# Performance work log

Hardware: AMD Instinct MI355X
Metric: run time of the kernel (lower is better)

The kernel has to match this reference:

```python
import jax, jax.numpy as jnp
import numpy as np

B, T, D = 2, 2048, 1280
H = 20
DH = D // H  # 64
S_PAST = 2048


def setup_inputs() -> dict:
    key = jax.random.key(0)
    ks = jax.random.split(key, 7)
    return {
        "x": jax.random.normal(ks[0], (B, T, D), dtype=jnp.float32),
        "past_K": jax.random.normal(ks[1], (B, H, S_PAST, DH), dtype=jnp.float32),
        "past_V": jax.random.normal(ks[2], (B, H, S_PAST, DH), dtype=jnp.float32),
        "w_q": jax.random.normal(ks[3], (D, D), dtype=jnp.float32),
        "w_k": jax.random.normal(ks[4], (D, D), dtype=jnp.float32),
        "w_v": jax.random.normal(ks[5], (D, D), dtype=jnp.float32),
        "W_o": jax.random.normal(ks[6], (D, D), dtype=jnp.float32),
    }


def reference(x, past_K, past_V, w_q, w_k, w_v, W_o):
    b, t, _ = x.shape
    # projections
    q = x @ w_q  # [B,T,D]
    k = x @ w_k
    v = x @ w_v
    # split heads -> [B,H,T,DH]
    Q = q.reshape(b, t, H, DH).transpose(0, 2, 1, 3)
    K = k.reshape(b, t, H, DH).transpose(0, 2, 1, 3)
    V = v.reshape(b, t, H, DH).transpose(0, 2, 1, 3)
    # concat KV cache along sequence dim
    K = jnp.concatenate([past_K, K], axis=-2)  # [B,H,S_past+T,DH]
    V = jnp.concatenate([past_V, V], axis=-2)
    # attention (no causal mask, matching the original module)
    scores = jnp.einsum("bhtd,bhsd->bhts", Q, K) / jnp.sqrt(jnp.float32(DH))
    attn = jax.nn.softmax(scores, axis=-1)
    values = jnp.einsum("bhts,bhsd->bhtd", attn, V)  # [B,H,T,DH]
    values = values.transpose(0, 2, 1, 3).reshape(b, t, D)
    out = values @ W_o
    return out, K, V
```

## Files before the change

### kernel.cpp

```cpp
#include <hip/hip_runtime.h>

#define NB 2
#define NH 20
#define TT 2048
#define DD 1280
#define DHH 64
#define SP 2048
#define SS 4096
#define MM (NB*TT)

typedef __attribute__((ext_vector_type(8))) short bf16x8;
typedef __attribute__((ext_vector_type(4))) float f32x4;
typedef unsigned short u16;
typedef unsigned int u32;

__device__ __forceinline__ f32x4 mfma16(bf16x8 a, bf16x8 b, f32x4 c) {
  return __builtin_amdgcn_mfma_f32_16x16x32_bf16(a, b, c, 0, 0, 0);
}

__device__ __forceinline__ u16 f2bf(float f) {
  u32 x = __builtin_bit_cast(u32, f);
  x += 0x7fffu + ((x >> 16) & 1u);
  return (u16)(x >> 16);
}
__device__ __forceinline__ float bf2f(u16 u) {
  u32 x = ((u32)u) << 16;
  return __builtin_bit_cast(float, x);
}

__device__ __forceinline__ float fexp2(float x) {
#if __has_builtin(__builtin_amdgcn_exp2f)
  return __builtin_amdgcn_exp2f(x);
#else
  return exp2f(x);
#endif
}

__device__ __forceinline__ u32 cvtpk(float lo, float hi) {
  u32 r;
  asm("v_cvt_pk_bf16_f32 %0, %1, %2" : "=v"(r) : "v"(lo), "v"(hi));
  return r;
}

__device__ __forceinline__ float vmax3(float a, float b, float c) {
  float d;
  asm("v_max3_f32 %0, %1, %2, %3" : "=v"(d) : "v"(a), "v"(b), "v"(c));
  return d;
}
__device__ __forceinline__ float max16(const f32x4* st) {
  float m0 = vmax3(st[0][0], st[0][1], st[0][2]);
  float m1 = vmax3(st[0][3], st[1][0], st[1][1]);
  float m2 = vmax3(st[1][2], st[1][3], st[2][0]);
  float m3 = vmax3(st[2][1], st[2][2], st[2][3]);
  float m4 = vmax3(st[3][0], st[3][1], st[3][2]);
  float m5 = vmax3(m0, m1, st[3][3]);
  float m6 = vmax3(m2, m3, m4);
  return fmaxf(m5, m6);
}

#define VMCNT0() asm volatile("s_waitcnt vmcnt(0)" ::: "memory")
#define BAR() __builtin_amdgcn_s_barrier()

template<int ROWS>
__device__ __forceinline__ void stage_swz(char* lds, const u16* __restrict__ gsrc,
                                          int ld, int tid) {
  constexpr int ITER = ROWS * 8 / 256;
#pragma unroll
  for (int i = 0; i < ITER; ++i) {
    int id = i * 256 + tid;
    int row = id >> 3, c = id & 7;
    int cs = c ^ (row & 7);
    const u16* src = gsrc + row * ld + cs * 8;
    __builtin_amdgcn_global_load_lds(
        (const __attribute__((address_space(1))) u32*)src,
        (__attribute__((address_space(3))) u32*)(lds + id * 16), 16, 0, 0);
  }
}

__device__ __forceinline__ void gload16(const u16* src, char* ldst) {
  __builtin_amdgcn_global_load_lds(
      (const __attribute__((address_space(1))) u32*)src,
      (__attribute__((address_space(3))) u32*)ldst, 16, 0, 0);
}

__device__ __forceinline__ bf16x8 frag_swz(const char* lds, int row, int cc) {
  return *(const bf16x8*)(lds + row * 128 + ((cc ^ (row & 7)) << 4));
}
__device__ __forceinline__ bf16x8 frag32(const char* lds, int row, int cc) {
  return *(const bf16x8*)(lds + row * 64 + ((cc ^ (row & 3)) << 4));
}

__global__ void splitx(const float* __restrict__ x, u16* __restrict__ xh,
                       u16* __restrict__ xl) {
  int i = blockIdx.x * 256 + threadIdx.x;
  float4 v = ((const float4*)x)[i];
  ushort4 hi, lo;
  hi.x = f2bf(v.x); lo.x = f2bf(v.x - bf2f(hi.x));
  hi.y = f2bf(v.y); lo.y = f2bf(v.y - bf2f(hi.y));
  hi.z = f2bf(v.z); lo.z = f2bf(v.z - bf2f(hi.z));
  hi.w = f2bf(v.w); lo.w = f2bf(v.w - bf2f(hi.w));
  ((ushort4*)xh)[i] = hi;
  ((ushort4*)xl)[i] = lo;
}

__global__ void transw(const float* __restrict__ wq, const float* __restrict__ wk,
                       const float* __restrict__ wv, const float* __restrict__ wo,
                       u16* __restrict__ wqkvh, u16* __restrict__ wqkvl,
                       u16* __restrict__ wot) {
  __shared__ float tile[64][65];
  int mat = blockIdx.z;
  const float* src = mat == 0 ? wq : mat == 1 ? wk : mat == 2 ? wv : wo;
  int k0 = blockIdx.x * 64, n0 = blockIdx.y * 64;
  int tid = threadIdx.x;
#pragma unroll
  for (int rep = 0; rep < 16; ++rep) {
    int id = rep * 256 + tid;
    int kl = id >> 6, nl = id & 63;
    tile[nl][kl] = src[(k0 + kl) * DD + n0 + nl];
  }
  __syncthreads();
#pragma unroll
  for (int rep = 0; rep < 16; ++rep) {
    int id = rep * 256 + tid;
    int nl = id >> 6, kl = id & 63;
    float v = tile[nl][kl];
    u16 hi = f2bf(v);
    if (mat < 3) {
      int idx = (mat * DD + n0 + nl) * DD + k0 + kl;
      wqkvh[idx] = hi;
      wqkvl[idx] = f2bf(v - bf2f(hi));
    } else {
      wot[(n0 + nl) * DD + k0 + kl] = hi;
    }
  }
}

__global__ void pastk(const float* __restrict__ pK, float* __restrict__ dK,
                      u16* __restrict__ Kh, u16* __restrict__ Kl) {
  int i = blockIdx.x * 256 + threadIdx.x;
  int e = i * 4;
  int dh = e & 63;
  int s = (e >> 6) & (SP - 1);
  int bh = e >> 17;
  float4 v = *(const float4*)(pK + e);
  int o = (bh * SS + s) * DHH + dh;
  *(float4*)(dK + o) = v;
  ushort4 hi, lo;
  hi.x = f2bf(v.x); lo.x = f2bf(v.x - bf2f(hi.x));
  hi.y = f2bf(v.y); lo.y = f2bf(v.y - bf2f(hi.y));
  hi.z = f2bf(v.z); lo.z = f2bf(v.z - bf2f(hi.z));
  hi.w = f2bf(v.w); lo.w = f2bf(v.w - bf2f(hi.w));
  *(ushort4*)(Kh + o) = hi;
  *(ushort4*)(Kl + o) = lo;
}

__global__ void pastv(const float* __restrict__ pV, float* __restrict__ dV,
                      u16* __restrict__ Vt) {
  __shared__ u16 tile[64][72];
  int bi = blockIdx.x;
  int bh = bi >> 5, st = bi & 31;
  int s0 = st * 64;
  int tid = threadIdx.x;
  const float* src = pV + (bh * SP + s0) * DHH;
  float* dst = dV + (bh * SS + s0) * DHH;
#pragma unroll
  for (int rep = 0; rep < 16; ++rep) {
    int id = rep * 256 + tid;
    int sl = id >> 6, dh = id & 63;
    float v = src[sl * DHH + dh];
    dst[sl * DHH + dh] = v;
    tile[dh][sl] = f2bf(v);
  }
  __syncthreads();
  u16* vdst = Vt + (bh * DHH) * SS + s0;
#pragma unroll
  for (int rep = 0; rep < 4; ++rep) {
    int id = rep * 256 + tid;
    int dh = id >> 4, s4 = (id & 15) * 4;
    ushort4 vv;
    vv.x = tile[dh][s4];     vv.y = tile[dh][s4 + 1];
    vv.z = tile[dh][s4 + 2]; vv.w = tile[dh][s4 + 3];
    *(ushort4*)(vdst + dh * SS + s4) = vv;
  }
}

__launch_bounds__(256, 2)
__global__ void gemm_qkv(const u16* __restrict__ xh, const u16* __restrict__ xl,
                         const u16* __restrict__ wh, const u16* __restrict__ wl,
                         u16* __restrict__ Qh, u16* __restrict__ Ql,
                         u16* __restrict__ Kh, u16* __restrict__ Kl,
                         u16* __restrict__ Vt,
                         float* __restrict__ dK, float* __restrict__ dV) {
  __shared__ __align__(16) char sm[65536];
  int tid = threadIdx.x, lane = tid & 63, w = tid >> 6;
  int wm = w >> 1, wn = w & 1;
  int r15 = lane & 15, grp = lane >> 4;
  int mBase = blockIdx.x * 128;
  int by = blockIdx.y;
  int nGlob = by * 128;
  const bool split = (by < 20);
  f32x4 acc[4][4] = {};
  int id0 = tid, id1 = 256 + tid;
  int r0 = id0 >> 2, c0 = id0 & 3;
  int r1 = id1 >> 2, c1 = id1 & 3;
  int so0 = r0 * DD + (c0 ^ (r0 & 3)) * 8;
  int so1 = r1 * DD + (c1 ^ (r1 & 3)) * 8;
  const u16* aH = xh + mBase * DD;
  const u16* aL = xl + mBase * DD;
  const u16* bH = wh + nGlob * DD;
  const u16* bL = wl + nGlob * DD;
  int do0 = id0 * 16, do1 = id1 * 16;

  auto stage = [&](int buf, int k0) {
    char* b = sm + buf * 32768;
    gload16(aH + k0 + so0, b + do0);
    gload16(aH + k0 + so1, b + do1);
    gload16(bH + k0 + so0, b + 16384 + do0);
    gload16(bH + k0 + so1, b + 16384 + do1);
    if (split) {
      gload16(aL + k0 + so0, b + 8192 + do0);
      gload16(aL + k0 + so1, b + 8192 + do1);
      gload16(bL + k0 + so0, b + 24576 + do0);
      gload16(bL + k0 + so1, b + 24576 + do1);
    }
  };
  auto compute = [&](int buf) {
    const char* b = sm + buf * 32768;
    bf16x8 fah[4], fal[4], fbh[4], fbl[4];
#pragma unroll
    for (int i = 0; i < 4; ++i) {
      fah[i] = frag32(b, wm * 64 + i * 16 + r15, grp);
      fbh[i] = frag32(b + 16384, wn * 64 + i * 16 + r15, grp);
      if (split) {
        fal[i] = frag32(b + 8192, wm * 64 + i * 16 + r15, grp);
        fbl[i] = frag32(b + 24576, wn * 64 + i * 16 + r15, grp);
      }
    }
    __builtin_amdgcn_s_setprio(1);
    if (split) {
#pragma unroll
      for (int i = 0; i < 4; ++i)
#pragma unroll
        for (int j = 0; j < 4; ++j) {
          acc[i][j] = mfma16(fah[i], fbh[j], acc[i][j]);
          acc[i][j] = mfma16(fah[i], fbl[j], acc[i][j]);
          acc[i][j] = mfma16(fal[i], fbh[j], acc[i][j]);
        }
    } else {
#pragma unroll
      for (int i = 0; i < 4; ++i)
#pragma unroll
        for (int j = 0; j < 4; ++j)
          acc[i][j] = mfma16(fah[i], fbh[j], acc[i][j]);
    }
    __builtin_amdgcn_s_setprio(0);
  };

  stage(0, 0);
  VMCNT0(); BAR();
#pragma unroll 2
  for (int step = 0; step < 39; ++step) {
    stage((step + 1) & 1, (step + 1) * 32);
    compute(step & 1);
    VMCNT0(); BAR();
  }
  compute(1);

  int proj = by / 10;
  int nb = (by % 10) * 128 + wn * 64;
#pragma unroll
  for (int i = 0; i < 4; ++i)
#pragma unroll
    for (int j = 0; j < 4; ++j)
#pragma unroll
      for (int r = 0; r < 4; ++r) {
        int m = mBase + wm * 64 + i * 16 + grp * 4 + r;
        int n = nb + j * 16 + r15;
        float v = acc[i][j][r];
        int b = m >> 11, t = m & 2047;
        int h = n >> 6, dh = n & 63;
        int bhh = b * NH + h;
        if (proj == 0) {
          float q = v * 0.180336880111f;
          u16 hi = f2bf(q);
          int idx = (bhh * TT + t) * DHH + dh;
          Qh[idx] = hi;
          Ql[idx] = f2bf(q - bf2f(hi));
        } else if (proj == 1) {
          int idx = (bhh * SS + SP + t) * DHH + dh;
          dK[idx] = v;
          u16 hi = f2bf(v);
          Kh[idx] = hi;
          Kl[idx] = f2bf(v - bf2f(hi));
        } else {
          int idx = (bhh * SS + SP + t) * DHH + dh;
          dV[idx] = v;
          Vt[(bhh * DHH + dh) * SS + SP + t] = f2bf(v);
        }
      }
}

__launch_bounds__(256, 3)
__global__ void attn(const u16* __restrict__ Qh, const u16* __restrict__ Ql,
                     const u16* __restrict__ Kh, const u16* __restrict__ Kl,
                     const u16* __restrict__ Vt, u16* __restrict__ ao) {
  __shared__ __align__(16) char Ks[8192];
  __shared__ __align__(16) char Kls[8192];
  __shared__ __align__(16) char Vs[8192];
  __shared__ __align__(16) u16 Pw[4][2][16][72];
  __shared__ __align__(16) float bc[4][16];
  int d = blockIdx.x;
  int xcd = d & 7, sl = d >> 3;
  int bh = xcd * 5 + (sl >> 4);
  int q0 = (sl & 15) * 128;
  int tid = threadIdx.x, lane = tid & 63, w = tid >> 6;
  int r15 = lane & 15, grp = lane >> 4;
  int qbase = q0 + w * 32;
  bf16x8 fqh[2][2], fql[2][2];
#pragma unroll
  for (int qt = 0; qt < 2; ++qt) {
    int qrow = qbase + qt * 16 + r15;
    const u16* qb = Qh + (bh * TT + qrow) * DHH + grp * 8;
    const u16* qbl = Ql + (bh * TT + qrow) * DHH + grp * 8;
    fqh[qt][0] = *(const bf16x8*)qb;   fqh[qt][1] = *(const bf16x8*)(qb + 32);
    fql[qt][0] = *(const bf16x8*)qbl;  fql[qt][1] = *(const bf16x8*)(qbl + 32);
  }
  float mrun[2] = {-1e30f, -1e30f};
  float lrun[2] = {0.f, 0.f};
  f32x4 oacc[2][4] = {};
  int id0 = tid, id1 = 256 + tid;
  int r0 = id0 >> 3, c0 = id0 & 7;
  int r1 = id1 >> 3, c1 = id1 & 7;
  const u16* kh0 = Kh + bh * SS * DHH + r0 * DHH + (c0 ^ (r0 & 7)) * 8;
  const u16* kh1 = Kh + bh * SS * DHH + r1 * DHH + (c1 ^ (r1 & 7)) * 8;
  const u16* kl0 = Kl + bh * SS * DHH + r0 * DHH + (c0 ^ (r0 & 7)) * 8;
  const u16* kl1 = Kl + bh * SS * DHH + r1 * DHH + (c1 ^ (r1 & 7)) * 8;
  const u16* v0 = Vt + bh * DHH * SS + r0 * SS + (c0 ^ (r0 & 7)) * 8;
  const u16* v1 = Vt + bh * DHH * SS + r1 * SS + (c1 ^ (r1 & 7)) * 8;
  char* dK0 = Ks + id0 * 16;  char* dK1 = Ks + id1 * 16;
  char* dL0 = Kls + id0 * 16; char* dL1 = Kls + id1 * 16;
  char* dV0 = Vs + id0 * 16;  char* dV1 = Vs + id1 * 16;

  for (int it = 0; it < SS / 64; ++it) {
    gload16(kh0, dK0); gload16(kh1, dK1);
    gload16(kl0, dL0); gload16(kl1, dL1);
    gload16(v0, dV0);  gload16(v1, dV1);
    kh0 += 64 * DHH; kh1 += 64 * DHH;
    kl0 += 64 * DHH; kl1 += 64 * DHH;
    v0 += 64; v1 += 64;
    __syncthreads();
    f32x4 st[2][4];
    __builtin_amdgcn_s_setprio(1);
#pragma unroll
    for (int kt = 0; kt < 4; ++kt) {
      bf16x8 k0f = frag_swz(Ks, kt * 16 + r15, grp);
      bf16x8 k1f = frag_swz(Ks, kt * 16 + r15, 4 + grp);
#pragma unroll
      for (int qt = 0; qt < 2; ++qt) {
        f32x4 a = {0.f, 0.f, 0.f, 0.f};
        a = mfma16(k0f, fqh[qt][0], a);
        a = mfma16(k1f, fqh[qt][1], a);
        st[qt][kt] = a;
      }
    }
    __builtin_amdgcn_s_setprio(0);
    float cm[2];
#pragma unroll
    for (int qt = 0; qt < 2; ++qt) {
      float c = max16(st[qt]);
      c = fmaxf(c, __shfl_xor(c, 16));
      c = fmaxf(c, __shfl_xor(c, 32));
      cm[qt] = c;
    }
    bool act = (!__all(cm[0] <= mrun[0] - 88.f)) |
               (!__all(cm[1] <= mrun[1] - 88.f));
    if (act) {
      __builtin_amdgcn_s_setprio(1);
#pragma unroll
      for (int kt = 0; kt < 4; ++kt) {
        bf16x8 k0f = frag_swz(Ks, kt * 16 + r15, grp);
        bf16x8 k1f = frag_swz(Ks, kt * 16 + r15, 4 + grp);
        bf16x8 l0f = frag_swz(Kls, kt * 16 + r15, grp);
        bf16x8 l1f = frag_swz(Kls, kt * 16 + r15, 4 + grp);
#pragma unroll
        for (int qt = 0; qt < 2; ++qt) {
          st[qt][kt] = mfma16(l0f, fqh[qt][0], st[qt][kt]);
          st[qt][kt] = mfma16(k0f, fql[qt][0], st[qt][kt]);
          st[qt][kt] = mfma16(l1f, fqh[qt][1], st[qt][kt]);
          st[qt][kt] = mfma16(k1f, fql[qt][1], st[qt][kt]);
        }
      }
      __builtin_amdgcn_s_setprio(0);
#pragma unroll
      for (int qt = 0; qt < 2; ++qt) {
        if (!__all(cm[qt] <= mrun[qt] + 8.f)) {
          float mnew = fmaxf(mrun[qt], cm[qt]);
          float sc = fexp2(mrun[qt] - mnew);
          lrun[qt] *= sc;
          mrun[qt] = mnew;
          if (grp == 0) bc[w][r15] = sc;
          f32x4 scv = *(const f32x4*)&bc[w][grp * 4];
#pragma unroll
          for (int dd = 0; dd < 4; ++dd) {
            oacc[qt][dd][0] *= scv[0]; oacc[qt][dd][1] *= scv[1];
            oacc[qt][dd][2] *= scv[2]; oacc[qt][dd][3] *= scv[3];
          }
        }
        float m = mrun[qt];
        float ps = 0.f;
#pragma unroll
        for (int kt = 0; kt < 4; ++kt)
#pragma unroll
          for (int r = 0; r < 4; ++r) {
            float p = fexp2(st[qt][kt][r] - m);
            st[qt][kt][r] = p;
            ps += p;
          }
        ps += __shfl_xor(ps, 16);
        ps += __shfl_xor(ps, 32);
        lrun[qt] += ps;
#pragma unroll
        for (int kt = 0; kt < 4; ++kt) {
          u32 w0 = cvtpk(st[qt][kt][0], st[qt][kt][1]);
          u32 w1 = cvtpk(st[qt][kt][2], st[qt][kt][3]);
          uint2 pk = {w0, w1};
          *(uint2*)&Pw[w][qt][r15][kt * 16 + grp * 4] = pk;
        }
      }
      bf16x8 pa[2][2];
#pragma unroll
      for (int qt = 0; qt < 2; ++qt) {
        pa[qt][0] = *(const bf16x8*)&Pw[w][qt][r15][grp * 8];
        pa[qt][1] = *(const bf16x8*)&Pw[w][qt][r15][32 + grp * 8];
      }
      __builtin_amdgcn_s_setprio(1);
#pragma unroll
      for (int dd = 0; dd < 4; ++dd) {
        bf16x8 vf0 = frag_swz(Vs, dd * 16 + r15, grp);
        bf16x8 vf1 = frag_swz(Vs, dd * 16 + r15, 4 + grp);
#pragma unroll
        for (int qt = 0; qt < 2; ++qt) {
          oacc[qt][dd] = mfma16(pa[qt][0], vf0, oacc[qt][dd]);
          oacc[qt][dd] = mfma16(pa[qt][1], vf1, oacc[qt][dd]);
        }
      }
      __builtin_amdgcn_s_setprio(0);
    }
    __syncthreads();
  }
  int b = bh / NH, h = bh % NH;
#pragma unroll
  for (int qt = 0; qt < 2; ++qt) {
    float inv = 1.0f / lrun[qt];
    if (grp == 0) bc[w][r15] = inv;
    f32x4 li = *(const f32x4*)&bc[w][grp * 4];
#pragma unroll
    for (int dd = 0; dd < 4; ++dd)
#pragma unroll
      for (int r = 0; r < 4; ++r) {
        int q = qbase + qt * 16 + grp * 4 + r;
        int col = h * DHH + dd * 16 + r15;
        ao[(b * TT + q) * DD + col] = f2bf(oacc[qt][dd][r] * li[r]);
      }
  }
}

__launch_bounds__(256, 2)
__global__ void gemm_out(const u16* __restrict__ ao, const u16* __restrict__ wot,
                         float* __restrict__ out) {
  __shared__ __align__(16) char sm[32768];
  char* As = sm;
  char* Bs = sm + 16384;
  int tid = threadIdx.x, lane = tid & 63, w = tid >> 6;
  int wm = w >> 1, wn = w & 1;
  int r15 = lane & 15, grp = lane >> 4;
  int mBase = blockIdx.x * 128, nBase = blockIdx.y * 128;
  f32x4 acc[4][4] = {};
  for (int k0 = 0; k0 < DD; k0 += 64) {
    stage_swz<128>(As, ao + mBase * DD + k0, DD, tid);
    stage_swz<128>(Bs, wot + nBase * DD + k0, DD, tid);
    __syncthreads();
#pragma unroll
    for (int kk = 0; kk < 2; ++kk) {
      int cc = kk * 4 + grp;
      bf16x8 fa[4], fb[4];
#pragma unroll
      for (int i = 0; i < 4; ++i) {
        fa[i] = frag_swz(As, wm * 64 + i * 16 + r15, cc);
        fb[i] = frag_swz(Bs, wn * 64 + i * 16 + r15, cc);
      }
#pragma unroll
      for (int i = 0; i < 4; ++i)
#pragma unroll
        for (int j = 0; j < 4; ++j)
          acc[i][j] = mfma16(fa[i], fb[j], acc[i][j]);
    }
    __syncthreads();
  }
#pragma unroll
  for (int i = 0; i < 4; ++i)
#pragma unroll
    for (int j = 0; j < 4; ++j)
#pragma unroll
      for (int r = 0; r < 4; ++r) {
        int m = mBase + wm * 64 + i * 16 + grp * 4 + r;
        int n = nBase + wn * 64 + j * 16 + r15;
        out[m * DD + n] = acc[i][j][r];
      }
}

extern "C" void kernel_launch(void* const* d_in, const int* in_sizes, int n_in,
                              void* d_out, int out_size, void* d_ws, size_t ws_size,
                              hipStream_t stream) {
  const float* x  = (const float*)d_in[0];
  const float* pK = (const float*)d_in[1];
  const float* pV = (const float*)d_in[2];
  const float* wq = (const float*)d_in[3];
  const float* wk = (const float*)d_in[4];
  const float* wv = (const float*)d_in[5];
  const float* wo = (const float*)d_in[6];

  float* out = (float*)d_out;
  float* dK  = out + NB * TT * DD;
  float* dV  = dK + NB * NH * SS * DHH;

  u16* xh    = (u16*)d_ws;
  u16* xl    = xh + MM * DD;
  u16* wqkvh = xl + MM * DD;
  u16* wqkvl = wqkvh + 3 * DD * DD;
  u16* wot   = wqkvl + 3 * DD * DD;
  u16* Qh    = wot + DD * DD;
  u16* Ql    = Qh + MM * DD;
  u16* Kh    = Ql + MM * DD;
  u16* Kl    = Kh + NB * NH * SS * DHH;
  u16* Vt    = Kl + NB * NH * SS * DHH;
  u16* ao    = xh;

  splitx<<<dim3(MM * DD / 4 / 256), 256, 0, stream>>>(x, xh, xl);
  transw<<<dim3(20, 20, 4), 256, 0, stream>>>(wq, wk, wv, wo, wqkvh, wqkvl, wot);
  pastk<<<dim3(NB * NH * SP * DHH / 4 / 256), 256, 0, stream>>>(pK, dK, Kh, Kl);
  pastv<<<dim3(NB * NH * (SP / 64)), 256, 0, stream>>>(pV, dV, Vt);
  gemm_qkv<<<dim3(32, 30), 256, 0, stream>>>(xh, xl, wqkvh, wqkvl,
                                             Qh, Ql, Kh, Kl, Vt, dK, dV);
  attn<<<dim3(NB * NH * (TT / 128)), 256, 0, stream>>>(Qh, Ql, Kh, Kl, Vt, ao);
  gemm_out<<<dim3(32, 10), 256, 0, stream>>>(ao, wot, out);
}
```

Measured before the change: 377.6 us.

## Double-buffer output-projection GEMM with 32-wide K steps and raise occupancy

Rewrites the output projection GEMM to stage 32-wide K slices into two LDS buffers, so the next slice's global-to-LDS load is issued before the current slice's MFMAs. Each step needs one barrier instead of two. It also raises launch bounds to 3 blocks per CU and wraps the MFMA burst in s_setprio. Halving the K tile doubles the number of barrier iterations, and the higher occupancy target may limit registers.

Result: no change. 378.0 us (median of 3 runs) (+0.1%).

```diff
diff --git a/kernel.cpp b/kernel.cpp
--- a/kernel.cpp
+++ b/kernel.cpp
@@ -60,22 +60,6 @@
 
 #define VMCNT0() asm volatile("s_waitcnt vmcnt(0)" ::: "memory")
 #define BAR() __builtin_amdgcn_s_barrier()
-
-template<int ROWS>
-__device__ __forceinline__ void stage_swz(char* lds, const u16* __restrict__ gsrc,
-                                          int ld, int tid) {
-  constexpr int ITER = ROWS * 8 / 256;
-#pragma unroll
-  for (int i = 0; i < ITER; ++i) {
-    int id = i * 256 + tid;
-    int row = id >> 3, c = id & 7;
-    int cs = c ^ (row & 7);
-    const u16* src = gsrc + row * ld + cs * 8;
-    __builtin_amdgcn_global_load_lds(
-        (const __attribute__((address_space(1))) u32*)src,
-        (__attribute__((address_space(3))) u32*)(lds + id * 16), 16, 0, 0);
-  }
-}
 
 __device__ __forceinline__ void gload16(const u16* src, char* ldst) {
   __builtin_amdgcn_global_load_lds(
@@ -465,38 +449,58 @@
   }
 }
 
-__launch_bounds__(256, 2)
+__launch_bounds__(256, 3)
 __global__ void gemm_out(const u16* __restrict__ ao, const u16* __restrict__ wot,
                          float* __restrict__ out) {
   __shared__ __align__(16) char sm[32768];
-  char* As = sm;
-  char* Bs = sm + 16384;
   int tid = threadIdx.x, lane = tid & 63, w = tid >> 6;
   int wm = w >> 1, wn = w & 1;
   int r15 = lane & 15, grp = lane >> 4;
   int mBase = blockIdx.x * 128, nBase = blockIdx.y * 128;
   f32x4 acc[4][4] = {};
-  for (int k0 = 0; k0 < DD; k0 += 64) {
-    stage_swz<128>(As, ao + mBase * DD + k0, DD, tid);
-    stage_swz<128>(Bs, wot + nBase * DD + k0, DD, tid);
-    __syncthreads();
-#pragma unroll
-    for (int kk = 0; kk < 2; ++kk) {
-      int cc = kk * 4 + grp;
-      bf16x8 fa[4], fb[4];
-#pragma unroll
-      for (int i = 0; i < 4; ++i) {
-        fa[i] = frag_swz(As, wm * 64 + i * 16 + r15, cc);
-        fb[i] = frag_swz(Bs, wn * 64 + i * 16 + r15, cc);
-      }
-#pragma unroll
-      for (int i = 0; i < 4; ++i)
-#pragma unroll
-        for (int j = 0; j < 4; ++j)
-          acc[i][j] = mfma16(fa[i], fb[j], acc[i][j]);
-    }
-    __syncthreads();
-  }
+  int id0 = tid, id1 = 256 + tid;
+  int r0 = id0 >> 2, c0 = id0 & 3;
+  int r1 = id1 >> 2, c1 = id1 & 3;
+  int so0 = r0 * DD + (c0 ^ (r0 & 3)) * 8;
+  int so1 = r1 * DD + (c1 ^ (r1 & 3)) * 8;
+  const u16* aP = ao + mBase * DD;
+  const u16* bP = wot + nBase * DD;
+  int do0 = id0 * 16, do1 = id1 * 16;
+
+  auto stage = [&](int buf, int k0) {
+    char* b = sm + buf * 16384;
+    gload16(aP + k0 + so0, b + do0);
+    gload16(aP + k0 + so1, b + do1);
+    gload16(bP + k0 + so0, b + 8192 + do0);
+    gload16(bP + k0 + so1, b + 8192 + do1);
+  };
+  auto compute = [&](int buf) {
+    const char* b = sm + buf * 16384;
+    bf16x8 fa[4], fb[4];
+#pragma unroll
+    for (int i = 0; i < 4; ++i) {
+      fa[i] = frag32(b, wm * 64 + i * 16 + r15, grp);
+      fb[i] = frag32(b + 8192, wn * 64 + i * 16 + r15, grp);
+    }
+    __builtin_amdgcn_s_setprio(1);
+#pragma unroll
+    for (int i = 0; i < 4; ++i)
+#pragma unroll
+      for (int j = 0; j < 4; ++j)
+        acc[i][j] = mfma16(fa[i], fb[j], acc[i][j]);
+    __builtin_amdgcn_s_setprio(0);
+  };
+
+  stage(0, 0);
+  VMCNT0(); BAR();
+#pragma unroll 2
+  for (int step = 0; step < 39; ++step) {
+    stage((step + 1) & 1, (step + 1) * 32);
+    compute(step & 1);
+    VMCNT0(); BAR();
+  }
+  compute(1);
+
 #pragma unroll
   for (int i = 0; i < 4; ++i)
 #pragma unroll
```
